# Performance work log

Hardware: AMD Instinct MI355X
Metric: run time of the kernel (lower is better)

Reference implementation:

```python
import jax, jax.numpy as jnp
import numpy as np

N = 50000   # nodes
E = 400000  # edges
IN_DIM, H1, H2, OUT_DIM = 512, 256, 62, 128


def _param(key, shape, scale=0.05):
    return jax.random.normal(key, shape, dtype=jnp.float32) * scale


def setup_inputs() -> dict:
    key = jax.random.key(0)
    ks = jax.random.split(key, 24)
    x = jax.random.normal(ks[0], (N, IN_DIM), dtype=jnp.float32)
    edge_index_neg = jax.random.randint(ks[1], (2, E), 0, N, dtype=jnp.int64)
    d = {
        "x": x, "edge_index_neg": edge_index_neg,
        # nn.Linear params (W stored as [in, out])
        "W1": _param(ks[2], (IN_DIM, H1)), "b1": _param(ks[3], (H1,)),
        "W2": _param(ks[4], (H1, H2)),    "b2": _param(ks[5], (H2,)),
        "W3": _param(ks[6], (H2, OUT_DIM)), "b3": _param(ks[7], (OUT_DIM,)),
        # GCNConv params: lin weight (no bias) + post-aggregation bias
        "Wg1": _param(ks[8], (H1, H1)),   "bg1": _param(ks[9], (H1,)),
        "Wg2": _param(ks[10], (H2, H2)),  "bg2": _param(ks[11], (H2,)),
        "Wg3": _param(ks[12], (OUT_DIM, OUT_DIM)), "bg3": _param(ks[13], (OUT_DIM,)),
        "Wg4": _param(ks[14], (OUT_DIM, OUT_DIM)), "bg4": _param(ks[15], (OUT_DIM,)),
        "Wg5": _param(ks[16], (OUT_DIM, OUT_DIM)), "bg5": _param(ks[17], (OUT_DIM,)),
        "Wg6": _param(ks[18], (OUT_DIM, OUT_DIM)), "bg6": _param(ks[19], (OUT_DIM,)),
    }
    return d


def _build_norm(edge_index):
    # PyG GCNConv: add self-loops, symmetric normalization D^-1/2 A D^-1/2
    loop = jnp.arange(N, dtype=edge_index.dtype)
    src = jnp.concatenate([edge_index[0], loop])
    dst = jnp.concatenate([edge_index[1], loop])
    deg = jax.ops.segment_sum(jnp.ones_like(dst, dtype=jnp.float32), dst, num_segments=N)
    dinv = jnp.where(deg > 0, jax.lax.rsqrt(jnp.maximum(deg, 1.0)), 0.0)
    norm = dinv[src] * dinv[dst]  # [E+N]
    return src, dst, norm


def _gcn(x, W, b, src, dst, norm):
    h = x @ W                                   # [N, F]
    msg = h[src] * norm[:, None]                # gather + edge scale
    out = jax.ops.segment_sum(msg, dst, num_segments=N)  # scatter-add
    return out + b


def reference(x, edge_index_neg, W1, b1, W2, b2, W3, b3,
              Wg1, bg1, Wg2, bg2, Wg3, bg3, Wg4, bg4, Wg5, bg5, Wg6, bg6):
    src, dst, norm = _build_norm(edge_index_neg)
    relu = jax.nn.relu
    x1l = x @ W1 + b1
    x1 = x1l + relu(_gcn(x1l, Wg1, bg1, src, dst, norm))
    x2l = x1 @ W2 + b2
    x2 = x2l + relu(_gcn(x2l, Wg2, bg2, src, dst, norm))
    x3l = x2 @ W3 + b3
    x3 = x3l + 0.5 * relu(_gcn(x3l, Wg3, bg3, src, dst, norm))
    x4 = x3 + 0.5 * relu(_gcn(x4_in := x3, Wg4, bg4, src, dst, norm))
    x5 = x4 + 0.25 * relu(_gcn(x4, Wg5, bg5, src, dst, norm))
    x6 = x5 + 0.25 * _gcn(x5, Wg6, bg6, src, dst, norm)
    return x6
```

## Files before the change

kernel.cpp:

```cpp
#include <hip/hip_runtime.h>

#define NN 50000
#define NE 400000
#define NBLK 196

using short8 = __attribute__((ext_vector_type(8))) short;
using f32x4  = __attribute__((ext_vector_type(4))) float;
using f32x2  = __attribute__((ext_vector_type(2))) float;
using u16x2  = __attribute__((ext_vector_type(2))) unsigned short;
using u16x4  = __attribute__((ext_vector_type(4))) unsigned short;

__device__ __forceinline__ unsigned short f2b(float f) {
    union { float f; unsigned int u; } x; x.f = f;
    unsigned int u = x.u;
    u += 0x7fffu + ((u >> 16) & 1u);
    return (unsigned short)(u >> 16);
}
__device__ __forceinline__ float b2f(unsigned short u) {
    union { unsigned int u; float f; } x; x.u = ((unsigned int)u) << 16;
    return x.f;
}

#define SWZ(b, row) ((b) ^ (((row) & 7) << 4))

__global__ __launch_bounds__(256) void zero2_k(int* a, int* b) {
    int i = blockIdx.x * 256 + threadIdx.x;
    if (i < NN) { a[i] = 0; b[i] = 0; }
}
__global__ __launch_bounds__(256) void count_k(const int* __restrict__ dst, int* __restrict__ indeg) {
    int e = blockIdx.x * 256 + threadIdx.x;
    if (e < NE) atomicAdd(&indeg[dst[e]], 1);
}
__global__ __launch_bounds__(256) void scan1_k(const int* __restrict__ indeg, int* __restrict__ tmp,
                                               int* __restrict__ bsum) {
    __shared__ int s[256];
    int t = threadIdx.x, i = blockIdx.x * 256 + t;
    int v = (i < NN) ? indeg[i] : 0;
    s[t] = v; __syncthreads();
    for (int off = 1; off < 256; off <<= 1) {
        int x = (t >= off) ? s[t - off] : 0;
        __syncthreads();
        s[t] += x;
        __syncthreads();
    }
    if (i < NN) tmp[i] = s[t];
    if (t == 255) bsum[blockIdx.x] = s[255];
}
__global__ __launch_bounds__(256) void scan2_k(const int* __restrict__ bsum, int* __restrict__ boff) {
    __shared__ int s[256];
    int t = threadIdx.x;
    int v = (t < NBLK) ? bsum[t] : 0;
    s[t] = v; __syncthreads();
    for (int off = 1; off < 256; off <<= 1) {
        int x = (t >= off) ? s[t - off] : 0;
        __syncthreads();
        s[t] += x;
        __syncthreads();
    }
    if (t < NBLK) boff[t] = s[t] - v;
}
__global__ __launch_bounds__(256) void scan3_k(const int* __restrict__ tmp, const int* __restrict__ indeg,
                                               const int* __restrict__ boff, int* __restrict__ rowptr,
                                               float* __restrict__ dinv) {
    int i = blockIdx.x * 256 + threadIdx.x;
    if (i < NN) {
        rowptr[i] = tmp[i] - indeg[i] + boff[i >> 8];
        dinv[i] = rsqrtf((float)(1 + indeg[i]));
    }
    if (i == 0) rowptr[NN] = NE;
}
__global__ __launch_bounds__(256) void fill_k(const int* __restrict__ src, const int* __restrict__ dst,
                                              const float* __restrict__ dinv, const int* __restrict__ rowptr,
                                              int* __restrict__ cursor, int2* __restrict__ ebn) {
    int e = blockIdx.x * 256 + threadIdx.x;
    if (e >= NE) return;
    int s = src[e], d = dst[e];
    int pos = atomicAdd(&cursor[d], 1);
    ebn[rowptr[d] + pos] = make_int2(s, __float_as_int(dinv[s] * dinv[d]));
}

struct WSegs {
    const float* W[9];
    unsigned short* Wt[9];
    int K[9], N[9], Kp[9];
    int c0[10];
};
__global__ __launch_bounds__(256) void wcast_all_k(WSegs s) {
    int blk = blockIdx.x;
    #pragma unroll
    for (int g = 0; g < 9; g++) {
        if (blk >= s.c0[g] && blk < s.c0[g + 1]) {
            int idx = (blk - s.c0[g]) * 256 + threadIdx.x;
            int Kp = s.Kp[g];
            int n = idx / Kp, k = idx % Kp;
            float v = (n < s.N[g] && k < s.K[g]) ? s.W[g][(size_t)k * s.N[g] + n] : 0.0f;
            s.Wt[g][idx] = f2b(v);
        }
    }
}

template<bool AF32, int BM, int BN>
__global__ __launch_bounds__(256) void gemm_mfma_k(
    const void* __restrict__ Araw, const unsigned short* __restrict__ Bt,
    const float* __restrict__ bias, unsigned short* __restrict__ C,
    int M, int lda, int Kp, int N, int ldc) {
    constexpr int MR = BM / 32;
    constexpr int NF = BN / 32;
    constexpr int nA = BM / 32;
    constexpr int nB = BN / 32;
    constexpr int BUFB = (BM + BN) * 128;
    __shared__ __align__(16) char lds[2 * BUFB];

    int tid = threadIdx.x;
    int lane = tid & 63, wave = tid >> 6;
    int wr = wave >> 1, wc = wave & 1;
    int lr = lane & 15, lk = lane >> 4;
    int r0 = blockIdx.x * BM, c0 = blockIdx.y * BN;

    f32x4 acc[MR][NF];
    #pragma unroll
    for (int m = 0; m < MR; m++)
        #pragma unroll
        for (int n = 0; n < NF; n++)
            acc[m][n] = (f32x4){0.f, 0.f, 0.f, 0.f};

    float4 fa0[nA], fa1[nA];
    short8 ra[nA], rb[nB];

    auto LOAD = [&](int k0) {
        #pragma unroll
        for (int c = 0; c < nA; c++) {
            int o = tid + c * 256, row = o >> 3, oct = o & 7;
            int gr = r0 + row;
            if constexpr (AF32) {
                if (gr < M) {
                    const float* p = (const float*)Araw + (size_t)gr * lda + k0 + oct * 8;
                    fa0[c] = *(const float4*)p;
                    fa1[c] = *(const float4*)(p + 4);
                } else {
                    fa0[c] = make_float4(0, 0, 0, 0);
                    fa1[c] = make_float4(0, 0, 0, 0);
                }
            } else {
                short8 z = {0, 0, 0, 0, 0, 0, 0, 0};
                ra[c] = (gr < M)
                    ? *(const short8*)((const unsigned short*)Araw + (size_t)gr * lda + k0 + oct * 8)
                    : z;
            }
        }
        #pragma unroll
        for (int c = 0; c < nB; c++) {
            int o = tid + c * 256, row = o >> 3, oct = o & 7;
            rb[c] = *(const short8*)(Bt + (size_t)(c0 + row) * Kp + k0 + oct * 8);
        }
    };
    auto STORE = [&](char* AsB, char* BsB) {
        #pragma unroll
        for (int c = 0; c < nA; c++) {
            int o = tid + c * 256, row = o >> 3, oct = o & 7;
            short8 v;
            if constexpr (AF32) {
                v[0] = (short)f2b(fa0[c].x); v[1] = (short)f2b(fa0[c].y);
                v[2] = (short)f2b(fa0[c].z); v[3] = (short)f2b(fa0[c].w);
                v[4] = (short)f2b(fa1[c].x); v[5] = (short)f2b(fa1[c].y);
                v[6] = (short)f2b(fa1[c].z); v[7] = (short)f2b(fa1[c].w);
            } else {
                v = ra[c];
            }
            *(short8*)(AsB + SWZ(row * 128 + oct * 16, row)) = v;
        }
        #pragma unroll
        for (int c = 0; c < nB; c++) {
            int o = tid + c * 256, row = o >> 3, oct = o & 7;
            *(short8*)(BsB + SWZ(row * 128 + oct * 16, row)) = rb[c];
        }
    };

    int nt = Kp >> 6;
    LOAD(0);
    STORE(lds, lds + BM * 128);
    __syncthreads();
    for (int t = 0; t < nt; t++) {
        char* cur = lds + (t & 1) * BUFB;
        char* alt = lds + ((t + 1) & 1) * BUFB;
        if (t + 1 < nt) LOAD((t + 1) << 6);
        char* AsB = cur;
        char* BsB = cur + BM * 128;
        #pragma unroll
        for (int kk = 0; kk < 2; kk++) {
            int kb = kk * 64 + lk * 16;
            short8 a[MR], b[NF];
            #pragma unroll
            for (int m = 0; m < MR; m++) {
                int row = wr * (BM / 2) + m * 16 + lr;
                a[m] = *(short8*)(AsB + SWZ(row * 128 + kb, row));
            }
            #pragma unroll
            for (int n = 0; n < NF; n++) {
                int row = wc * (BN / 2) + n * 16 + lr;
                b[n] = *(short8*)(BsB + SWZ(row * 128 + kb, row));
            }
            #pragma unroll
            for (int m = 0; m < MR; m++)
                #pragma unroll
                for (int n = 0; n < NF; n++)
                    acc[m][n] = __builtin_amdgcn_mfma_f32_16x16x32_bf16(a[m], b[n], acc[m][n], 0, 0, 0);
        }
        if (t + 1 < nt) STORE(alt, alt + BM * 128);
        __syncthreads();
    }

    constexpr int LDC = BN + 8;
    unsigned short* ldsC = (unsigned short*)lds;
    #pragma unroll
    for (int n = 0; n < NF; n++) {
        int cc = wc * (BN / 2) + n * 16 + lr;
        int gc = c0 + cc;
        float bv = (bias != nullptr && gc < N) ? bias[gc] : 0.0f;
        bool ok = gc < N;
        #pragma unroll
        for (int m = 0; m < MR; m++)
            #pragma unroll
            for (int j = 0; j < 4; j++) {
                int row = wr * (BM / 2) + m * 16 + lk * 4 + j;
                float v = ok ? acc[m][n][j] + bv : 0.0f;
                ldsC[row * LDC + cc] = f2b(v);
            }
    }
    __syncthreads();
    constexpr int CH = (BM * BN) / 2048;
    #pragma unroll
    for (int c = 0; c < CH; c++) {
        int o = tid + c * 256;
        int row = o / (BN / 8), col = (o % (BN / 8)) * 8;
        int gr = r0 + row;
        if (gr < M)
            *(short8*)(C + (size_t)gr * ldc + c0 + col) = *(short8*)(ldsC + row * LDC + col);
    }
}

template<int VEC> struct BV;
template<> struct BV<1> { using T = unsigned short; };
template<> struct BV<2> { using T = u16x2; };
template<> struct BV<4> { using T = u16x4; };
template<int VEC> struct FV;
template<> struct FV<1> { using T = float; };
template<> struct FV<2> { using T = f32x2; };
template<> struct FV<4> { using T = f32x4; };

template<int VEC, int SPLIT, bool OUTF32>
__global__ __launch_bounds__(256) void gather_k(
    const unsigned short* __restrict__ h, const unsigned short* __restrict__ base,
    const float* __restrict__ dinv, const float* __restrict__ bias,
    const int2* __restrict__ ebn, const int* __restrict__ rowptr,
    void* __restrict__ outraw, float alpha, int dorelu, int F) {
    constexpr int ld = 64 * VEC * SPLIT;
    int gw = (blockIdx.x * 256 + threadIdx.x) >> 6;
    int lane = threadIdx.x & 63;
    int w = gw / SPLIT;
    int colbase = (gw % SPLIT) * 64 * VEC;
    if (w >= NN) return;
    using LT = typename BV<VEC>::T;
    const int col = colbase + lane * VEC;

    float acc[VEC];
    float dn = dinv[w];
    {
        LT t = *(const LT*)(h + (size_t)w * ld + col);
        const unsigned short* tu = (const unsigned short*)&t;
        #pragma unroll
        for (int v = 0; v < VEC; v++) acc[v] = b2f(tu[v]) * dn * dn;
    }
    int e = rowptr[w], end = rowptr[w + 1];
    for (; e + 8 <= end; e += 8) {
        long long q[8];
        #pragma unroll
        for (int i = 0; i < 8; i++)
            q[i] = __builtin_nontemporal_load((const long long*)(ebn + e + i));
        LT t[8];
        #pragma unroll
        for (int i = 0; i < 8; i++)
            t[i] = *(const LT*)(h + (size_t)(int)q[i] * ld + col);
        #pragma unroll
        for (int i = 0; i < 8; i++) {
            float nr = __int_as_float((int)(q[i] >> 32));
            const unsigned short* u = (const unsigned short*)&t[i];
            #pragma unroll
            for (int v = 0; v < VEC; v++) acc[v] += b2f(u[v]) * nr;
        }
    }
    for (; e + 2 <= end; e += 2) {
        long long q0 = __builtin_nontemporal_load((const long long*)(ebn + e));
        long long q1 = __builtin_nontemporal_load((const long long*)(ebn + e + 1));
        LT t0 = *(const LT*)(h + (size_t)(int)q0 * ld + col);
        LT t1 = *(const LT*)(h + (size_t)(int)q1 * ld + col);
        float n0 = __int_as_float((int)(q0 >> 32)), n1 = __int_as_float((int)(q1 >> 32));
        const unsigned short* u0 = (const unsigned short*)&t0;
        const unsigned short* u1 = (const unsigned short*)&t1;
        #pragma unroll
        for (int v = 0; v < VEC; v++) acc[v] += b2f(u0[v]) * n0 + b2f(u1[v]) * n1;
    }
    if (e < end) {
        long long q0 = __builtin_nontemporal_load((const long long*)(ebn + e));
        LT t0 = *(const LT*)(h + (size_t)(int)q0 * ld + col);
        float n0 = __int_as_float((int)(q0 >> 32));
        const unsigned short* u0 = (const unsigned short*)&t0;
        #pragma unroll
        for (int v = 0; v < VEC; v++) acc[v] += b2f(u0[v]) * n0;
    }
    LT bt = *(const LT*)(base + (size_t)w * ld + col);
    const unsigned short* bu = (const unsigned short*)&bt;
    if (OUTF32) {
        typename FV<VEC>::T ot;
        float* of = (float*)&ot;
        #pragma unroll
        for (int v = 0; v < VEC; v++) {
            int f = col + v;
            float a = acc[v] + ((f < F) ? bias[f] : 0.0f);
            if (dorelu) a = fmaxf(a, 0.0f);
            of[v] = (f < F) ? b2f(bu[v]) + alpha * a : 0.0f;
        }
        *(typename FV<VEC>::T*)((float*)outraw + (size_t)w * ld + col) = ot;
    } else {
        LT ot;
        unsigned short* ou = (unsigned short*)&ot;
        #pragma unroll
        for (int v = 0; v < VEC; v++) {
            int f = col + v;
            float a = acc[v] + ((f < F) ? bias[f] : 0.0f);
            if (dorelu) a = fmaxf(a, 0.0f);
            float res = (f < F) ? b2f(bu[v]) + alpha * a : 0.0f;
            ou[v] = f2b(res);
        }
        *(LT*)((unsigned short*)outraw + (size_t)w * ld + col) = ot;
    }
}

extern "C" void kernel_launch(void* const* d_in, const int* in_sizes, int n_in,
                              void* d_out, int out_size, void* d_ws, size_t ws_size,
                              hipStream_t stream) {
    const float* x   = (const float*)d_in[0];
    const int*   ei  = (const int*)d_in[1];
    const float* W1  = (const float*)d_in[2];  const float* b1  = (const float*)d_in[3];
    const float* W2  = (const float*)d_in[4];  const float* b2  = (const float*)d_in[5];
    const float* W3  = (const float*)d_in[6];  const float* b3  = (const float*)d_in[7];
    const float* Wg1 = (const float*)d_in[8];  const float* bg1 = (const float*)d_in[9];
    const float* Wg2 = (const float*)d_in[10]; const float* bg2 = (const float*)d_in[11];
    const float* Wg3 = (const float*)d_in[12]; const float* bg3 = (const float*)d_in[13];
    const float* Wg4 = (const float*)d_in[14]; const float* bg4 = (const float*)d_in[15];
    const float* Wg5 = (const float*)d_in[16]; const float* bg5 = (const float*)d_in[17];
    const float* Wg6 = (const float*)d_in[18]; const float* bg6 = (const float*)d_in[19];
    const int* srcv = ei;
    const int* dstv = ei + NE;

    float* dinv = (float*)d_ws;
    unsigned short* hA = (unsigned short*)(dinv + 51200);
    unsigned short* hB = hA + (size_t)NN * 256;
    unsigned short* hC = hB + (size_t)NN * 256;
    unsigned short* W1t  = hC + (size_t)NN * 256;
    unsigned short* Wg1t = W1t  + 256 * 512;
    unsigned short* W2t  = Wg1t + 256 * 256;
    unsigned short* Wg2t = W2t  + 64 * 256;
    unsigned short* W3t  = Wg2t + 64 * 64;
    unsigned short* Wg3t = W3t  + 128 * 64;
    unsigned short* Wg4t = Wg3t + 128 * 128;
    unsigned short* Wg5t = Wg4t + 128 * 128;
    unsigned short* Wg6t = Wg5t + 128 * 128;
    int* indeg  = (int*)(Wg6t + 128 * 128);
    int* cursor = indeg + 51200;
    int* tmp    = cursor + 51200;
    int* rowptr = tmp + 51200;
    int* bsum   = rowptr + 51264;
    int* boff   = bsum + 256;
    int2* ebn   = (int2*)(boff + 256);

    zero2_k<<<NBLK, 256, 0, stream>>>(indeg, cursor);
    count_k<<<(NE + 255) / 256, 256, 0, stream>>>(dstv, indeg);
    scan1_k<<<NBLK, 256, 0, stream>>>(indeg, tmp, bsum);
    scan2_k<<<1, 256, 0, stream>>>(bsum, boff);
    scan3_k<<<NBLK, 256, 0, stream>>>(tmp, indeg, boff, rowptr, dinv);
    fill_k<<<(NE + 255) / 256, 256, 0, stream>>>(srcv, dstv, dinv, rowptr, cursor, ebn);

    {
        WSegs s;
        const float* Ws[9] = {W1, Wg1, W2, Wg2, W3, Wg3, Wg4, Wg5, Wg6};
        unsigned short* Wts[9] = {W1t, Wg1t, W2t, Wg2t, W3t, Wg3t, Wg4t, Wg5t, Wg6t};
        int Ks[9]  = {512, 256, 256, 62, 62, 128, 128, 128, 128};
        int Ns[9]  = {256, 256, 62, 62, 128, 128, 128, 128, 128};
        int Kps[9] = {512, 256, 256, 64, 64, 128, 128, 128, 128};
        int Nps[9] = {256, 256, 64, 64, 128, 128, 128, 128, 128};
        int c = 0;
        for (int g = 0; g < 9; g++) {
            s.W[g] = Ws[g]; s.Wt[g] = Wts[g];
            s.K[g] = Ks[g]; s.N[g] = Ns[g]; s.Kp[g] = Kps[g];
            s.c0[g] = c;
            c += (Kps[g] * Nps[g]) / 256;
        }
        s.c0[9] = c;
        wcast_all_k<<<c, 256, 0, stream>>>(s);
    }

    const int GX2 = (NN + 127) / 128;
    const int GG1 = (NN * 64 + 255) / 256;

    gemm_mfma_k<true, 128, 128><<<dim3(GX2, 2), 256, 0, stream>>>(x, W1t, b1, hA, NN, 512, 512, 256, 256);
    gemm_mfma_k<false, 128, 128><<<dim3(GX2, 2), 256, 0, stream>>>(hA, Wg1t, nullptr, hB, NN, 256, 256, 256, 256);
    gather_k<4, 1, false><<<GG1, 256, 0, stream>>>(hB, hA, dinv, bg1, ebn, rowptr, hC, 1.0f, 1, 256);
    gemm_mfma_k<false, 128, 64><<<dim3(GX2, 1), 256, 0, stream>>>(hC, W2t, b2, hA, NN, 256, 256, 62, 64);
    gemm_mfma_k<false, 128, 64><<<dim3(GX2, 1), 256, 0, stream>>>(hA, Wg2t, nullptr, hB, NN, 64, 64, 62, 64);
    gather_k<1, 1, false><<<GG1, 256, 0, stream>>>(hB, hA, dinv, bg2, ebn, rowptr, hC, 1.0f, 1, 62);
    gemm_mfma_k<false, 128, 128><<<dim3(GX2, 1), 256, 0, stream>>>(hC, W3t, b3, hA, NN, 64, 64, 128, 128);
    gemm_mfma_k<false, 128, 128><<<dim3(GX2, 1), 256, 0, stream>>>(hA, Wg3t, nullptr, hB, NN, 128, 128, 128, 128);
    gather_k<2, 1, false><<<GG1, 256, 0, stream>>>(hB, hA, dinv, bg3, ebn, rowptr, hC, 0.5f, 1, 128);
    gemm_mfma_k<false, 128, 128><<<dim3(GX2, 1), 256, 0, stream>>>(hC, Wg4t, nullptr, hA, NN, 128, 128, 128, 128);
    gather_k<2, 1, false><<<GG1, 256, 0, stream>>>(hA, hC, dinv, bg4, ebn, rowptr, hB, 0.5f, 1, 128);
    gemm_mfma_k<false, 128, 128><<<dim3(GX2, 1), 256, 0, stream>>>(hB, Wg5t, nullptr, hA, NN, 128, 128, 128, 128);
    gather_k<2, 1, false><<<GG1, 256, 0, stream>>>(hA, hB, dinv, bg5, ebn, rowptr, hC, 0.25f, 1, 128);
    gemm_mfma_k<false, 128, 128><<<dim3(GX2, 1), 256, 0, stream>>>(hC, Wg6t, nullptr, hA, NN, 128, 128, 128, 128);
    gather_k<2, 1, true><<<GG1, 256, 0, stream>>>(hA, hC, dinv, bg6, ebn, rowptr, d_out, 0.25f, 0, 128);
}
```

Before: 392.0 us.

## Use full-width 128x256 tile GEMM for the 256-column layers

Adds a 512-thread GEMM kernel that covers all 256 output columns per block, and uses it for the first two GEMMs instead of launching the 128x128 kernel over two column blocks. Each A row tile is now read from global memory once instead of twice, which halves A traffic, most notably for the 512-wide fp32 input x. The cost is a larger LDS footprint (about 96KB double-buffered), 64 accumulator registers per thread, and half as many blocks, all of which may lower occupancy.

```diff
diff --git a/kernel.cpp b/kernel.cpp
--- a/kernel.cpp
+++ b/kernel.cpp
@@ -96,6 +96,135 @@
             float v = (n < s.N[g] && k < s.K[g]) ? s.W[g][(size_t)k * s.N[g] + n] : 0.0f;
             s.Wt[g][idx] = f2b(v);
         }
+    }
+}
+
+template<bool AF32>
+__global__ __launch_bounds__(512) void gemm_wide_k(
+    const void* __restrict__ Araw, const unsigned short* __restrict__ Bt,
+    const float* __restrict__ bias, unsigned short* __restrict__ C,
+    int M, int lda, int Kp) {
+    constexpr int BM = 128, BN = 256;
+    constexpr int nA = 2;
+    constexpr int nB = 4;
+    constexpr int BUFB = (BM + BN) * 128;
+    __shared__ __align__(16) char lds[2 * BUFB];
+
+    int tid = threadIdx.x;
+    int lane = tid & 63, wave = tid >> 6;
+    int wr = wave >> 2, wc = wave & 3;
+    int lr = lane & 15, lk = lane >> 4;
+    int r0 = blockIdx.x * BM;
+
+    f32x4 acc[4][4];
+    #pragma unroll
+    for (int m = 0; m < 4; m++)
+        #pragma unroll
+        for (int n = 0; n < 4; n++)
+            acc[m][n] = (f32x4){0.f, 0.f, 0.f, 0.f};
+
+    float4 fa0[nA], fa1[nA];
+    short8 ra[nA], rb[nB];
+
+    auto LOAD = [&](int k0) {
+        #pragma unroll
+        for (int c = 0; c < nA; c++) {
+            int o = tid + c * 512, row = o >> 3, oct = o & 7;
+            int gr = min(r0 + row, M - 1);
+            if constexpr (AF32) {
+                const float* p = (const float*)Araw + (size_t)gr * lda + k0 + oct * 8;
+                fa0[c] = *(const float4*)p;
+                fa1[c] = *(const float4*)(p + 4);
+            } else {
+                ra[c] = *(const short8*)((const unsigned short*)Araw + (size_t)gr * lda + k0 + oct * 8);
+            }
+        }
+        #pragma unroll
+        for (int c = 0; c < nB; c++) {
+            int o = tid + c * 512, row = o >> 3, oct = o & 7;
+            rb[c] = *(const short8*)(Bt + (size_t)row * Kp + k0 + oct * 8);
+        }
+    };
+    auto STORE = [&](char* buf) {
+        char* AsB = buf;
+        char* BsB = buf + BM * 128;
+        #pragma unroll
+        for (int c = 0; c < nA; c++) {
+            int o = tid + c * 512, row = o >> 3, oct = o & 7;
+            short8 v;
+            if constexpr (AF32) {
+                v[0] = (short)f2b(fa0[c].x); v[1] = (short)f2b(fa0[c].y);
+                v[2] = (short)f2b(fa0[c].z); v[3] = (short)f2b(fa0[c].w);
+                v[4] = (short)f2b(fa1[c].x); v[5] = (short)f2b(fa1[c].y);
+                v[6] = (short)f2b(fa1[c].z); v[7] = (short)f2b(fa1[c].w);
+            } else {
+                v = ra[c];
+            }
+            *(short8*)(AsB + SWZ(row * 128 + oct * 16, row)) = v;
+        }
+        #pragma unroll
+        for (int c = 0; c < nB; c++) {
+            int o = tid + c * 512, row = o >> 3, oct = o & 7;
+            *(short8*)(BsB + SWZ(row * 128 + oct * 16, row)) = rb[c];
+        }
+    };
+
+    int nt = Kp >> 6;
+    LOAD(0);
+    STORE(lds);
+    __syncthreads();
+    for (int t = 0; t < nt; t++) {
+        char* cur = lds + (t & 1) * BUFB;
+        char* alt = lds + ((t + 1) & 1) * BUFB;
+        if (t + 1 < nt) LOAD((t + 1) << 6);
+        char* AsB = cur;
+        char* BsB = cur + BM * 128;
+        #pragma unroll
+        for (int kk = 0; kk < 2; kk++) {
+            int kb = kk * 64 + lk * 16;
+            short8 a[4], b[4];
+            #pragma unroll
+            for (int m = 0; m < 4; m++) {
+                int row = wr * 64 + m * 16 + lr;
+                a[m] = *(short8*)(AsB + SWZ(row * 128 + kb, row));
+            }
+            #pragma unroll
+            for (int n = 0; n < 4; n++) {
+                int row = wc * 64 + n * 16 + lr;
+                b[n] = *(short8*)(BsB + SWZ(row * 128 + kb, row));
+            }
+            #pragma unroll
+            for (int m = 0; m < 4; m++)
+                #pragma unroll
+                for (int n = 0; n < 4; n++)
+                    acc[m][n] = __builtin_amdgcn_mfma_f32_16x16x32_bf16(a[m], b[n], acc[m][n], 0, 0, 0);
+        }
+        if (t + 1 < nt) STORE(alt);
+        __syncthreads();
+    }
+
+    constexpr int LDC = BN + 8;
+    unsigned short* ldsC = (unsigned short*)lds;
+    #pragma unroll
+    for (int n = 0; n < 4; n++) {
+        int gc = wc * 64 + n * 16 + lr;
+        float bv = (bias != nullptr) ? bias[gc] : 0.0f;
+        #pragma unroll
+        for (int m = 0; m < 4; m++)
+            #pragma unroll
+            for (int j = 0; j < 4; j++) {
+                int row = wr * 64 + m * 16 + lk * 4 + j;
+                ldsC[row * LDC + gc] = f2b(acc[m][n][j] + bv);
+            }
+    }
+    __syncthreads();
+    #pragma unroll
+    for (int c = 0; c < 8; c++) {
+        int o = tid + c * 512;
+        int row = o >> 5, col = (o & 31) * 8;
+        int gr = r0 + row;
+        if (gr < M)
+            *(short8*)(C + (size_t)gr * 256 + col) = *(short8*)(ldsC + row * LDC + col);
     }
 }
 
@@ -403,8 +532,8 @@
     const int GX2 = (NN + 127) / 128;
     const int GG1 = (NN * 64 + 255) / 256;
 
-    gemm_mfma_k<true, 128, 128><<<dim3(GX2, 2), 256, 0, stream>>>(x, W1t, b1, hA, NN, 512, 512, 256, 256);
-    gemm_mfma_k<false, 128, 128><<<dim3(GX2, 2), 256, 0, stream>>>(hA, Wg1t, nullptr, hB, NN, 256, 256, 256, 256);
+    gemm_wide_k<true><<<GX2, 512, 0, stream>>>(x, W1t, b1, hA, NN, 512, 512);
+    gemm_wide_k<false><<<GX2, 512, 0, stream>>>(hA, Wg1t, nullptr, hB, NN, 256, 256);
     gather_k<4, 1, false><<<GG1, 256, 0, stream>>>(hB, hA, dinv, bg1, ebn, rowptr, hC, 1.0f, 1, 256);
     gemm_mfma_k<false, 128, 64><<<dim3(GX2, 1), 256, 0, stream>>>(hC, W2t, b2, hA, NN, 256, 256, 62, 64);
     gemm_mfma_k<false, 128, 64><<<dim3(GX2, 1), 256, 0, stream>>>(hA, Wg2t, nullptr, hB, NN, 64, 64, 62, 64);
```

New measurement: 372.9 us. 1.05x faster.

## Fuse back-to-back GEMM pairs per row block and merge zeroing into weight cast

Applied to the files above, without the earlier changes.

Consecutive dense GEMMs (x@W1 then @Wg1, W2 then Wg2, W3 then Wg3) now run in one kernel per 128-row block. The second GEMM reads the first's output, which the same block just wrote, so that data is likely still in cache, and two launches become one. The first pair uses 512-thread blocks with a full 256-wide N tile. The zeroing kernel is folded into the weight-cast kernel to save another launch. Out-of-range rows are now clamped instead of zero-filled. The larger LDS and register footprint may lower occupancy, and 391 blocks on 512 threads may underfill the GPU.

```diff
diff --git a/kernel.cpp b/kernel.cpp
--- a/kernel.cpp
+++ b/kernel.cpp
@@ -23,10 +23,6 @@
 
 #define SWZ(b, row) ((b) ^ (((row) & 7) << 4))
 
-__global__ __launch_bounds__(256) void zero2_k(int* a, int* b) {
-    int i = blockIdx.x * 256 + threadIdx.x;
-    if (i < NN) { a[i] = 0; b[i] = 0; }
-}
 __global__ __launch_bounds__(256) void count_k(const int* __restrict__ dst, int* __restrict__ indeg) {
     int e = blockIdx.x * 256 + threadIdx.x;
     if (e < NE) atomicAdd(&indeg[dst[e]], 1);
@@ -84,9 +80,15 @@
     unsigned short* Wt[9];
     int K[9], N[9], Kp[9];
     int c0[10];
+    int* z1; int* z2;
 };
-__global__ __launch_bounds__(256) void wcast_all_k(WSegs s) {
+__global__ __launch_bounds__(256) void wcast_zero_k(WSegs s) {
     int blk = blockIdx.x;
+    if (blk >= s.c0[9]) {
+        int i = (blk - s.c0[9]) * 256 + threadIdx.x;
+        if (i < NN) { s.z1[i] = 0; s.z2[i] = 0; }
+        return;
+    }
     #pragma unroll
     for (int g = 0; g < 9; g++) {
         if (blk >= s.c0[g] && blk < s.c0[g + 1]) {
@@ -99,27 +101,28 @@
     }
 }
 
-template<bool AF32, int BM, int BN>
-__global__ __launch_bounds__(256) void gemm_mfma_k(
-    const void* __restrict__ Araw, const unsigned short* __restrict__ Bt,
-    const float* __restrict__ bias, unsigned short* __restrict__ C,
-    int M, int lda, int Kp, int N, int ldc) {
-    constexpr int MR = BM / 32;
-    constexpr int NF = BN / 32;
-    constexpr int nA = BM / 32;
-    constexpr int nB = BN / 32;
+template<bool AF32, int BN, int NT>
+__device__ __forceinline__ void gemm_body(
+    const void* __restrict__ Araw, int lda, int Kp,
+    const unsigned short* __restrict__ Bt, const float* __restrict__ bias,
+    unsigned short* __restrict__ C, int N, int ldc, int M, int r0, char* lds) {
+    constexpr int BM = 128;
+    constexpr int NW = NT / 64;
+    constexpr int WC = NW / 2;
+    constexpr int WBN = BN / WC;
+    constexpr int NF = WBN / 16;
+    constexpr int nA = (BM * 8) / NT;
+    constexpr int nB = (BN * 8) / NT;
     constexpr int BUFB = (BM + BN) * 128;
-    __shared__ __align__(16) char lds[2 * BUFB];
 
     int tid = threadIdx.x;
     int lane = tid & 63, wave = tid >> 6;
-    int wr = wave >> 1, wc = wave & 1;
+    int wr = wave / WC, wc = wave % WC;
     int lr = lane & 15, lk = lane >> 4;
-    int r0 = blockIdx.x * BM, c0 = blockIdx.y * BN;
-
-    f32x4 acc[MR][NF];
+
+    f32x4 acc[4][NF];
     #pragma unroll
-    for (int m = 0; m < MR; m++)
+    for (int m = 0; m < 4; m++)
         #pragma unroll
         for (int n = 0; n < NF; n++)
             acc[m][n] = (f32x4){0.f, 0.f, 0.f, 0.f};
@@ -130,34 +133,28 @@
     auto LOAD = [&](int k0) {
         #pragma unroll
         for (int c = 0; c < nA; c++) {
-            int o = tid + c * 256, row = o >> 3, oct = o & 7;
-            int gr = r0 + row;
+            int o = tid + c * NT, row = o >> 3, oct = o & 7;
+            int gr = min(r0 + row, M - 1);
             if constexpr (AF32) {
-                if (gr < M) {
-                    const float* p = (const float*)Araw + (size_t)gr * lda + k0 + oct * 8;
-                    fa0[c] = *(const float4*)p;
-                    fa1[c] = *(const float4*)(p + 4);
-                } else {
-                    fa0[c] = make_float4(0, 0, 0, 0);
-                    fa1[c] = make_float4(0, 0, 0, 0);
-                }
+                const float* p = (const float*)Araw + (size_t)gr * lda + k0 + oct * 8;
+                fa0[c] = *(const float4*)p;
+                fa1[c] = *(const float4*)(p + 4);
             } else {
-                short8 z = {0, 0, 0, 0, 0, 0, 0, 0};
-                ra[c] = (gr < M)
-                    ? *(const short8*)((const unsigned short*)Araw + (size_t)gr * lda + k0 + oct * 8)
-                    : z;
+                ra[c] = *(const short8*)((const unsigned short*)Araw + (size_t)gr * lda + k0 + oct * 8);
             }
         }
         #pragma unroll
         for (int c = 0; c < nB; c++) {
-            int o = tid + c * 256, row = o >> 3, oct = o & 7;
-            rb[c] = *(const short8*)(Bt + (size_t)(c0 + row) * Kp + k0 + oct * 8);
+            int o = tid + c * NT, row = o >> 3, oct = o & 7;
+            rb[c] = *(const short8*)(Bt + (size_t)row * Kp + k0 + oct * 8);
         }
     };
-    auto STORE = [&](char* AsB, char* BsB) {
+    auto STORE = [&](char* buf) {
+        char* AsB = buf;
+        char* BsB = buf + BM * 128;
         #pragma unroll
         for (int c = 0; c < nA; c++) {
-            int o = tid + c * 256, row = o >> 3, oct = o & 7;
+            int o = tid + c * NT, row = o >> 3, oct = o & 7;
             short8 v;
             if constexpr (AF32) {
                 v[0] = (short)f2b(fa0[c].x); v[1] = (short)f2b(fa0[c].y);
@@ -171,14 +168,14 @@
         }
         #pragma unroll
         for (int c = 0; c < nB; c++) {
-            int o = tid + c * 256, row = o >> 3, oct = o & 7;
+            int o = tid + c * NT, row = o >> 3, oct = o & 7;
             *(short8*)(BsB + SWZ(row * 128 + oct * 16, row)) = rb[c];
         }
     };
 
     int nt = Kp >> 6;
     LOAD(0);
-    STORE(lds, lds + BM * 128);
+    STORE(lds);
     __syncthreads();
     for (int t = 0; t < nt; t++) {
         char* cur = lds + (t & 1) * BUFB;
@@ -189,24 +186,24 @@
         #pragma unroll
         for (int kk = 0; kk < 2; kk++) {
             int kb = kk * 64 + lk * 16;
-            short8 a[MR], b[NF];
+            short8 a[4], b[NF];
             #pragma unroll
-            for (int m = 0; m < MR; m++) {
-                int row = wr * (BM / 2) + m * 16 + lr;
+            for (int m = 0; m < 4; m++) {
+                int row = wr * 64 + m * 16 + lr;
                 a[m] = *(short8*)(AsB + SWZ(row * 128 + kb, row));
             }
             #pragma unroll
             for (int n = 0; n < NF; n++) {
-                int row = wc * (BN / 2) + n * 16 + lr;
+                int row = wc * WBN + n * 16 + lr;
                 b[n] = *(short8*)(BsB + SWZ(row * 128 + kb, row));
             }
             #pragma unroll
-            for (int m = 0; m < MR; m++)
+            for (int m = 0; m < 4; m++)
                 #pragma unroll
                 for (int n = 0; n < NF; n++)
                     acc[m][n] = __builtin_amdgcn_mfma_f32_16x16x32_bf16(a[m], b[n], acc[m][n], 0, 0, 0);
         }
-        if (t + 1 < nt) STORE(alt, alt + BM * 128);
+        if (t + 1 < nt) STORE(alt);
         __syncthreads();
     }
 
@@ -214,29 +211,59 @@
     unsigned short* ldsC = (unsigned short*)lds;
     #pragma unroll
     for (int n = 0; n < NF; n++) {
-        int cc = wc * (BN / 2) + n * 16 + lr;
-        int gc = c0 + cc;
+        int gc = wc * WBN + n * 16 + lr;
         float bv = (bias != nullptr && gc < N) ? bias[gc] : 0.0f;
         bool ok = gc < N;
         #pragma unroll
-        for (int m = 0; m < MR; m++)
+        for (int m = 0; m < 4; m++)
             #pragma unroll
             for (int j = 0; j < 4; j++) {
-                int row = wr * (BM / 2) + m * 16 + lk * 4 + j;
+                int row = wr * 64 + m * 16 + lk * 4 + j;
                 float v = ok ? acc[m][n][j] + bv : 0.0f;
-                ldsC[row * LDC + cc] = f2b(v);
+                ldsC[row * LDC + gc] = f2b(v);
             }
     }
     __syncthreads();
-    constexpr int CH = (BM * BN) / 2048;
+    constexpr int CH = (BM * BN / 8) / NT;
     #pragma unroll
     for (int c = 0; c < CH; c++) {
-        int o = tid + c * 256;
+        int o = tid + c * NT;
         int row = o / (BN / 8), col = (o % (BN / 8)) * 8;
         int gr = r0 + row;
         if (gr < M)
-            *(short8*)(C + (size_t)gr * ldc + c0 + col) = *(short8*)(ldsC + row * LDC + col);
-    }
+            *(short8*)(C + (size_t)gr * ldc + col) = *(short8*)(ldsC + row * LDC + col);
+    }
+}
+
+__global__ __launch_bounds__(512) void fused_wide_k(
+    const float* __restrict__ x, const unsigned short* __restrict__ W1t, const float* __restrict__ b1,
+    unsigned short* __restrict__ C1, const unsigned short* __restrict__ Wg1t,
+    unsigned short* __restrict__ C2, int M) {
+    __shared__ __align__(16) char lds[2 * (128 + 256) * 128];
+    int r0 = blockIdx.x * 128;
+    gemm_body<true, 256, 512>(x, 512, 512, W1t, b1, C1, 256, 256, M, r0, lds);
+    __syncthreads();
+    gemm_body<false, 256, 512>(C1, 256, 256, Wg1t, nullptr, C2, 256, 256, M, r0, lds);
+}
+
+template<int BN>
+__global__ __launch_bounds__(256) void fused_pair_k(
+    const unsigned short* __restrict__ A1, int lda1, int Kp1,
+    const unsigned short* __restrict__ B1t, const float* __restrict__ b1,
+    unsigned short* __restrict__ C1, int N,
+    const unsigned short* __restrict__ B2t, unsigned short* __restrict__ C2, int M) {
+    __shared__ __align__(16) char lds[2 * (128 + BN) * 128];
+    int r0 = blockIdx.x * 128;
+    gemm_body<false, BN, 256>(A1, lda1, Kp1, B1t, b1, C1, N, BN, M, r0, lds);
+    __syncthreads();
+    gemm_body<false, BN, 256>(C1, BN, BN, B2t, nullptr, C2, N, BN, M, r0, lds);
+}
+
+__global__ __launch_bounds__(256) void gemm128_k(
+    const unsigned short* __restrict__ A, const unsigned short* __restrict__ Bt,
+    unsigned short* __restrict__ C, int M) {
+    __shared__ __align__(16) char lds[2 * (128 + 128) * 128];
+    gemm_body<false, 128, 256>(A, 128, 128, Bt, nullptr, C, 128, 128, M, blockIdx.x * 128, lds);
 }
 
 template<int VEC> struct BV;
@@ -374,13 +401,7 @@
     int* boff   = bsum + 256;
     int2* ebn   = (int2*)(boff + 256);
 
-    zero2_k<<<NBLK, 256, 0, stream>>>(indeg, cursor);
-    count_k<<<(NE + 255) / 256, 256, 0, stream>>>(dstv, indeg);
-    scan1_k<<<NBLK, 256, 0, stream>>>(indeg, tmp, bsum);
-    scan2_k<<<1, 256, 0, stream>>>(bsum, boff);
-    scan3_k<<<NBLK, 256, 0, stream>>>(tmp, indeg, boff, rowptr, dinv);
-    fill_k<<<(NE + 255) / 256, 256, 0, stream>>>(srcv, dstv, dinv, rowptr, cursor, ebn);
-
+    int wc_blocks;
     {
         WSegs s;
         const float* Ws[9] = {W1, Wg1, W2, Wg2, W3, Wg3, Wg4, Wg5, Wg6};
@@ -397,25 +418,29 @@
             c += (Kps[g] * Nps[g]) / 256;
         }
         s.c0[9] = c;
-        wcast_all_k<<<c, 256, 0, stream>>>(s);
-    }
+        s.z1 = indeg; s.z2 = cursor;
+        wc_blocks = c + NBLK;
+        wcast_zero_k<<<wc_blocks, 256, 0, stream>>>(s);
+    }
+    count_k<<<(NE + 255) / 256, 256, 0, stream>>>(dstv, indeg);
+    scan1_k<<<NBLK, 256, 0, stream>>>(indeg, tmp, bsum);
+    scan2_k<<<1, 256, 0, stream>>>(bsum, boff);
+    scan3_k<<<NBLK, 256, 0, stream>>>(tmp, indeg, boff, rowptr, dinv);
+    fill_k<<<(NE + 255) / 256, 256, 0, stream>>>(srcv, dstv, dinv, rowptr, cursor, ebn);
 
     const int GX2 = (NN + 127) / 128;
     const int GG1 = (NN * 64 + 255) / 256;
 
-    gemm_mfma_k<true, 128, 128><<<dim3(GX2, 2), 256, 0, stream>>>(x, W1t, b1, hA, NN, 512, 512, 256, 256);
-    gemm_mfma_k<false, 128, 128><<<dim3(GX2, 2), 256, 0, stream>>>(hA, Wg1t, nullptr, hB, NN, 256, 256, 256, 256);
+    fused_wide_k<<<GX2, 512, 0, stream>>>(x, W1t, b1, hA, Wg1t, hB, NN);
     gather_k<4, 1, false><<<GG1, 256, 0, stream>>>(hB, hA, dinv, bg1, ebn, rowptr, hC, 1.0f, 1, 256);
-    gemm_mfma_k<false, 128, 64><<<dim3(GX2, 1), 256, 0, stream>>>(hC, W2t, b2, hA, NN, 256, 256, 62, 64);
-    gemm_mfma_k<false, 128, 64><<<dim3(GX2, 1), 256, 0, stream>>>(hA, Wg2t, nullptr, hB, NN, 64, 64, 62, 64);
+    fused_pair_k<64><<<GX2, 256, 0, stream>>>(hC, 256, 256, W2t, b2, hA, 62, Wg2t, hB, NN);
     gather_k<1, 1, false><<<GG1, 256, 0, stream>>>(hB, hA, dinv, bg2, ebn, rowptr, hC, 1.0f, 1, 62);
-    gemm_mfma_k<false, 128, 128><<<dim3(GX2, 1), 256, 0, stream>>>(hC, W3t, b3, hA, NN, 64, 64, 128, 128);
-    gemm_mfma_k<false, 128, 128><<<dim3(GX2, 1), 256, 0, stream>>>(hA, Wg3t, nullptr, hB, NN, 128, 128, 128, 128);
+    fused_pair_k<128><<<GX2, 256, 0, stream>>>(hC, 64, 64, W3t, b3, hA, 128, Wg3t, hB, NN);
     gather_k<2, 1, false><<<GG1, 256, 0, stream>>>(hB, hA, dinv, bg3, ebn, rowptr, hC, 0.5f, 1, 128);
-    gemm_mfma_k<false, 128, 128><<<dim3(GX2, 1), 256, 0, stream>>>(hC, Wg4t, nullptr, hA, NN, 128, 128, 128, 128);
+    gemm128_k<<<GX2, 256, 0, stream>>>(hC, Wg4t, hA, NN);
     gather_k<2, 1, false><<<GG1, 256, 0, stream>>>(hA, hC, dinv, bg4, ebn, rowptr, hB, 0.5f, 1, 128);
-    gemm_mfma_k<false, 128, 128><<<dim3(GX2, 1), 256, 0, stream>>>(hB, Wg5t, nullptr, hA, NN, 128, 128, 128, 128);
+    gemm128_k<<<GX2, 256, 0, stream>>>(hB, Wg5t, hA, NN);
     gather_k<2, 1, false><<<GG1, 256, 0, stream>>>(hA, hB, dinv, bg5, ebn, rowptr, hC, 0.25f, 1, 128);
-    gemm_mfma_k<false, 128, 128><<<dim3(GX2, 1), 256, 0, stream>>>(hC, Wg6t, nullptr, hA, NN, 128, 128, 128, 128);
+    gemm128_k<<<GX2, 256, 0, stream>>>(hC, Wg6t, hA, NN);
     gather_k<2, 1, true><<<GG1, 256, 0, stream>>>(hA, hC, dinv, bg6, ebn, rowptr, d_out, 0.25f, 0, 128);
 }
```

Result: faster. 361.1 us (-7.9%).
